# Kernel tuning notes

Hardware: AMD Instinct MI355X
Metric: run time of the kernel (lower is better)

Reference implementation:

```python
import jax, jax.numpy as jnp
import numpy as np

NUM_HEADS = 4
NUM_GROUPS = 8
EPS = 1e-5


def group_norm(x, w, b):
    # x: [B, C, H, W], 8 groups, per-channel affine
    B, C, H, W = x.shape
    g = x.reshape(B, NUM_GROUPS, C // NUM_GROUPS, H, W)
    mu = g.mean(axis=(2, 3, 4), keepdims=True)
    var = g.var(axis=(2, 3, 4), keepdims=True)
    g = (g - mu) * jax.lax.rsqrt(var + EPS)
    x = g.reshape(B, C, H, W)
    return x * w[None, :, None, None] + b[None, :, None, None]


def setup_inputs() -> dict:
    key = jax.random.key(0)
    ks = jax.random.split(key, 7)
    B, C, H, W = 16, 256, 32, 32
    x = jax.random.normal(ks[0], (B, C, H, W), dtype=jnp.float32)
    norm_w = jnp.ones((C,), jnp.float32)
    norm_b = jnp.zeros((C,), jnp.float32)
    # 1x1 convs == channel matmuls; fan-in scaled init
    qkv_w = jax.random.normal(ks[1], (3 * C, C), dtype=jnp.float32) / np.sqrt(C)
    qkv_b = jnp.zeros((3 * C,), jnp.float32)
    proj_w = jax.random.normal(ks[2], (C, C), dtype=jnp.float32) / np.sqrt(C)
    proj_b = jnp.zeros((C,), jnp.float32)
    return {"x": x, "norm_w": norm_w, "norm_b": norm_b,
            "qkv_w": qkv_w, "qkv_b": qkv_b,
            "proj_w": proj_w, "proj_b": proj_b}


def reference(x, norm_w, norm_b, qkv_w, qkv_b, proj_w, proj_b):
    B, C, H, W = x.shape
    nh = NUM_HEADS
    d = C // nh
    N = H * W

    h = group_norm(x, norm_w, norm_b)
    # 1x1 conv -> channel matmul: [B, 3C, H, W]
    qkv = jnp.einsum('oc,bchw->bohw', qkv_w, h) + qkv_b[None, :, None, None]
    qkv = qkv.reshape(B, 3, nh, d, N)
    q, k, v = qkv[:, 0], qkv[:, 1], qkv[:, 2]  # [B, nh, d, N]

    scale = d ** (-0.5)
    attn = jnp.einsum('bhcn,bhcm->bhnm', q, k) * scale  # [B, nh, N, N]
    attn = jax.nn.softmax(attn, axis=-1)
    out = jnp.einsum('bhnm,bhcm->bhcn', attn, v)  # [B, nh, d, N]
    out = out.reshape(B, C, H, W)
    out = jnp.einsum('oc,bchw->bohw', proj_w, out) + proj_b[None, :, None, None]
    return x + out
```

## Files before the change

kernel.cpp:

```cpp
#include <hip/hip_runtime.h>
#include <math.h>

#define BATCH 16
#define CH 256
#define NG 8
#define NH 4
#define HD 64
#define NN 1024
#define GSZ 32
#define GELEMS (GSZ * NN)

typedef __attribute__((ext_vector_type(8))) __bf16 bf16x8;
typedef __attribute__((ext_vector_type(4))) __bf16 bf16x4;
typedef __attribute__((ext_vector_type(4))) _Float16 f16x4;
typedef __attribute__((ext_vector_type(4))) float f32x4;

__device__ __forceinline__ unsigned short f2b(float f) {
    union { __bf16 h; unsigned short u; } c; c.h = (__bf16)f; return c.u;
}
__device__ __forceinline__ unsigned short f2h(float f) {
    union { _Float16 h; unsigned short u; } c; c.h = (_Float16)f; return c.u;
}

#define MFMA(a, b, c) __builtin_amdgcn_mfma_f32_16x16x32_bf16(a, b, c, 0, 0, 0)
#define MFMA16(a, b, c) __builtin_amdgcn_mfma_f32_16x16x16f16(a, b, c, 0, 0, 0)

__global__ __launch_bounds__(256) void gnw_kernel(
    const float* __restrict__ x, const float* __restrict__ w,
    const float* __restrict__ bb, const float* __restrict__ qkv_w,
    const float* __restrict__ proj_w, unsigned short* __restrict__ hT,
    unsigned short* __restrict__ wq, unsigned short* __restrict__ wp)
{
    int tid = threadIdx.x;
    if (blockIdx.x >= 128) {
        int t = (blockIdx.x - 128) * 256 + tid;
        const float* src; unsigned short* dst; size_t off;
        if (t < 24576) { src = qkv_w; dst = wq; off = (size_t)t * 8; }
        else           { src = proj_w; dst = wp; off = (size_t)(t - 24576) * 8; }
        const float4* s4 = (const float4*)(src + off);
        float4 a = s4[0], b = s4[1];
        bf16x8 pk;
        pk[0] = (__bf16)a.x; pk[1] = (__bf16)a.y; pk[2] = (__bf16)a.z; pk[3] = (__bf16)a.w;
        pk[4] = (__bf16)b.x; pk[5] = (__bf16)b.y; pk[6] = (__bf16)b.z; pk[7] = (__bf16)b.w;
        *(bf16x8*)(dst + off) = pk;
        return;
    }
    const int b = blockIdx.x >> 3, g = blockIdx.x & 7;
    const float* xb = x + ((size_t)b * CH + g * GSZ) * NN;
    const float4* x4 = (const float4*)xb;

    float s = 0.f, ss = 0.f;
    #pragma unroll
    for (int i = 0; i < 32; ++i) {
        float4 v = x4[tid + i * 256];
        s  += v.x + v.y + v.z + v.w;
        ss += v.x * v.x + v.y * v.y + v.z * v.z + v.w * v.w;
    }
    #pragma unroll
    for (int off = 1; off < 64; off <<= 1) {
        s  += __shfl_xor(s, off);
        ss += __shfl_xor(ss, off);
    }
    __shared__ float red[8];
    int wave = tid >> 6, lane = tid & 63;
    if (lane == 0) { red[wave] = s; red[4 + wave] = ss; }
    __syncthreads();
    if (tid == 0) {
        float ts  = red[0] + red[1] + red[2] + red[3];
        float tss = red[4] + red[5] + red[6] + red[7];
        float mu  = ts * (1.f / GELEMS);
        float var = tss * (1.f / GELEMS) - mu * mu;
        red[0] = mu; red[1] = rsqrtf(var + 1e-5f);
    }
    __syncthreads();
    const float mu = red[0], rs = red[1];

    const int co = tid & 3;
    float wcv[8], bcv[8];
    #pragma unroll
    for (int j = 0; j < 8; ++j) {
        int c = g * GSZ + co * 8 + j;
        wcv[j] = w[c] * rs;
        bcv[j] = bb[c] - mu * wcv[j];
    }
    __shared__ float Ts[32][66];
    const int cs = tid >> 3, q = tid & 7;
    const int n_l = tid >> 2;
    for (int nt = 0; nt < 16; ++nt) {
        const float2* src = (const float2*)(xb + (size_t)cs * NN + nt * 64 + q * 8);
        #pragma unroll
        for (int t = 0; t < 4; ++t)
            *(float2*)&Ts[cs][q * 8 + t * 2] = src[t];
        __syncthreads();
        bf16x8 pk;
        #pragma unroll
        for (int j = 0; j < 8; ++j)
            pk[j] = (__bf16)(Ts[co * 8 + j][n_l] * wcv[j] + bcv[j]);
        *(bf16x8*)(hT + ((size_t)b * NN + nt * 64 + n_l) * CH + g * GSZ + co * 8) = pk;
        __syncthreads();
    }
}

template <int KIND>
__global__ __launch_bounds__(256) void gemm_kernel(
    const unsigned short* __restrict__ AT,
    const unsigned short* __restrict__ Wb,
    const float* __restrict__ bias,
    unsigned short* __restrict__ outT, unsigned short* __restrict__ outV,
    const float* __restrict__ res, float* __restrict__ out)
{
    __shared__ __align__(16) unsigned short Ws[64][136];
    __shared__ __align__(16) unsigned short Hs[64][136];
    const int b = blockIdx.z, o0 = blockIdx.y * 64, n0 = blockIdx.x * 64;
    const int tid = threadIdx.x;
    const int lane = tid & 63, wv = tid >> 6;
    const int l = lane & 15, quad = lane >> 4;
    const int iw = wv & 1, jw = wv >> 1;
    const bool qk_mode = (KIND == 0) && (blockIdx.y < 8);
    const bool v_mode  = (KIND == 0) && (blockIdx.y >= 8);
    const int r4 = tid >> 2, c4 = tid & 3;

    f32x4 acc[2][2] = {};
    for (int st = 0; st < 2; ++st) {
        const int cc0 = st * 128;
        #pragma unroll
        for (int i = 0; i < 4; ++i) {
            int ch = c4 + i * 4;
            *(bf16x8*)&Ws[r4][ch * 8] =
                *(const bf16x8*)(Wb + (size_t)(o0 + r4) * CH + cc0 + ch * 8);
            *(bf16x8*)&Hs[r4][ch * 8] =
                *(const bf16x8*)(AT + ((size_t)b * NN + n0 + r4) * CH + cc0 + ch * 8);
        }
        __syncthreads();
        #pragma unroll
        for (int kt = 0; kt < 4; ++kt) {
            bf16x8 af[2], bf[2];
            #pragma unroll
            for (int i = 0; i < 2; ++i)
                af[i] = *(const bf16x8*)&Hs[iw * 32 + i * 16 + l][kt * 32 + quad * 8];
            #pragma unroll
            for (int j = 0; j < 2; ++j)
                bf[j] = *(const bf16x8*)&Ws[jw * 32 + j * 16 + l][kt * 32 + quad * 8];
            #pragma unroll
            for (int i = 0; i < 2; ++i)
                #pragma unroll
                for (int j = 0; j < 2; ++j)
                    acc[i][j] = v_mode ? MFMA(af[i], bf[j], acc[i][j])
                                       : MFMA(bf[j], af[i], acc[i][j]);
        }
        __syncthreads();
    }

    unsigned short* Cs = (unsigned short*)Ws;
    if (qk_mode) {
        #pragma unroll
        for (int i = 0; i < 2; ++i)
            #pragma unroll
            for (int j = 0; j < 2; ++j) {
                int o_p = jw * 32 + j * 16 + quad * 4;
                int n_l = iw * 32 + i * 16 + l;
                bf16x4 pk;
                #pragma unroll
                for (int r = 0; r < 4; ++r)
                    pk[r] = (__bf16)(acc[i][j][r] + bias[o0 + o_p + r]);
                *(bf16x4*)&Cs[n_l * 72 + o_p] = pk;
            }
        __syncthreads();
        int rr = tid >> 2, ch = tid & 3;
        bf16x8 a0 = *(const bf16x8*)&Cs[rr * 72 + ch * 16];
        bf16x8 a1 = *(const bf16x8*)&Cs[rr * 72 + ch * 16 + 8];
        unsigned short* dst = outT + ((size_t)b * NN + n0 + rr) * 512 + o0 + ch * 16;
        *(bf16x8*)dst = a0;
        *(bf16x8*)(dst + 8) = a1;
    } else if (v_mode) {
        #pragma unroll
        for (int i = 0; i < 2; ++i)
            #pragma unroll
            for (int j = 0; j < 2; ++j) {
                int n_p = iw * 32 + i * 16 + quad * 4;
                int o_l = jw * 32 + j * 16 + l;
                float bs = bias[o0 + o_l];
                f16x4 pk;
                #pragma unroll
                for (int r = 0; r < 4; ++r)
                    pk[r] = (_Float16)(acc[i][j][r] + bs);
                *(f16x4*)&Cs[o_l * 72 + n_p] = pk;
            }
        __syncthreads();
        int rr = tid >> 2, ch = tid & 3;
        bf16x8 a0 = *(const bf16x8*)&Cs[rr * 72 + ch * 16];
        bf16x8 a1 = *(const bf16x8*)&Cs[rr * 72 + ch * 16 + 8];
        unsigned short* dst = outV + ((size_t)b * CH + (o0 + rr - 512)) * NN + n0 + ch * 16;
        *(bf16x8*)dst = a0;
        *(bf16x8*)(dst + 8) = a1;
    } else {
        #pragma unroll
        for (int i = 0; i < 2; ++i)
            #pragma unroll
            for (int j = 0; j < 2; ++j) {
                int o = o0 + jw * 32 + j * 16 + quad * 4;
                int n = n0 + iw * 32 + i * 16 + l;
                #pragma unroll
                for (int r = 0; r < 4; ++r) {
                    size_t idx = ((size_t)b * CH + o + r) * NN + n;
                    out[idx] = acc[i][j][r] + bias[o + r] + res[idx];
                }
            }
    }
}

__global__ __launch_bounds__(256, 4) void attn_kernel(
    const unsigned short* __restrict__ qkvT,
    const unsigned short* __restrict__ vbuf,
    unsigned short* __restrict__ ctxT)
{
    __shared__ __align__(16) unsigned short KV[2][8192];
    __shared__ float Lred[2][32];
    const int id = blockIdx.x;
    const int bh = id & 63, nt = id >> 6;
    const int b = bh >> 2, hh = bh & 3;
    const int n0 = nt * 64;
    const int tid = threadIdx.x;
    const int lane = tid & 63, w = tid >> 6;
    const int l = lane & 15, quad = lane >> 4;
    const int qx = w & 1, ky = w >> 1;
    const float KL2E = 0.125f * 1.44269504f;
    const int r4 = tid >> 2, c4 = tid & 3;

    bf16x8 qf[2][2];
    {
        const unsigned short* qp = qkvT + ((size_t)b * NN + n0 + 32 * qx + l) * 512 + hh * 64;
        #pragma unroll
        for (int ns = 0; ns < 2; ++ns)
            #pragma unroll
            for (int kt = 0; kt < 2; ++kt)
                qf[ns][kt] = *(const bf16x8*)(qp + (size_t)ns * 16 * 512 + kt * 32 + quad * 8);
    }

    const unsigned short* gk = qkvT + ((size_t)b * NN + r4) * 512 + 256 + hh * 64;
    const unsigned short* gv = vbuf + ((size_t)b * CH + hh * 64 + r4) * NN;
    const int p0 = (c4 ^ (r4 & 7)) * 8, p1 = ((c4 + 4) ^ (r4 & 7)) * 8;

    bf16x8 kpre0, kpre1, vpre0, vpre1;
    kpre0 = *(const bf16x8*)(gk + c4 * 8);
    kpre1 = *(const bf16x8*)(gk + (c4 + 4) * 8);
    vpre0 = *(const bf16x8*)(gv + c4 * 8);
    vpre1 = *(const bf16x8*)(gv + (c4 + 4) * 8);
    *(bf16x8*)&KV[0][r4 * 64 + p0] = kpre0;
    *(bf16x8*)&KV[0][r4 * 64 + p1] = kpre1;
    *(bf16x8*)&KV[0][4096 + r4 * 64 + p0] = vpre0;
    *(bf16x8*)&KV[0][4096 + r4 * 64 + p1] = vpre1;
    __syncthreads();

    float l_w[2] = {0.f, 0.f};
    f32x4 oacc[2][4] = {};

    for (int mt = 0; mt < 16; ++mt) {
        const int cur = mt & 1;
        if (mt < 15) {
            const unsigned short* gk1 = gk + (size_t)(mt + 1) * 64 * 512;
            const unsigned short* gv1 = gv + (mt + 1) * 64;
            kpre0 = *(const bf16x8*)(gk1 + c4 * 8);
            kpre1 = *(const bf16x8*)(gk1 + (c4 + 4) * 8);
            vpre0 = *(const bf16x8*)(gv1 + c4 * 8);
            vpre1 = *(const bf16x8*)(gv1 + (c4 + 4) * 8);
        }

        bf16x8 kf[2][2];
        #pragma unroll
        for (int mt2 = 0; mt2 < 2; ++mt2)
            #pragma unroll
            for (int kt = 0; kt < 2; ++kt)
                kf[mt2][kt] = *(const bf16x8*)
                    &KV[cur][(32 * ky + 16 * mt2 + l) * 64 + (((kt * 4 + quad) ^ (l & 7)) * 8)];

        f32x4 sacc[2][2] = {};
        #pragma unroll
        for (int kt = 0; kt < 2; ++kt)
            #pragma unroll
            for (int mt2 = 0; mt2 < 2; ++mt2)
                #pragma unroll
                for (int ns = 0; ns < 2; ++ns)
                    sacc[mt2][ns] = MFMA(kf[mt2][kt], qf[ns][kt], sacc[mt2][ns]);

        f16x4 pf[2][2];
        #pragma unroll
        for (int mt2 = 0; mt2 < 2; ++mt2)
            #pragma unroll
            for (int ns = 0; ns < 2; ++ns)
                #pragma unroll
                for (int r = 0; r < 4; ++r) {
                    float p = exp2f(sacc[mt2][ns][r] * KL2E);
                    l_w[ns] += p;
                    pf[mt2][ns][r] = (_Float16)p;
                }

        #pragma unroll
        for (int mt2 = 0; mt2 < 2; ++mt2) {
            const int q8 = 4 * ky + 2 * mt2 + (quad >> 1);
            const int vo = ((q8 ^ (l & 7)) * 8) + (quad & 1) * 4;
            #pragma unroll
            for (int ct = 0; ct < 4; ++ct) {
                f16x4 va = *(const f16x4*)&KV[cur][4096 + (16 * ct + l) * 64 + vo];
                #pragma unroll
                for (int ns = 0; ns < 2; ++ns)
                    oacc[ns][ct] = MFMA16(va, pf[mt2][ns], oacc[ns][ct]);
            }
        }

        if (mt < 15) {
            const int nxt = cur ^ 1;
            *(bf16x8*)&KV[nxt][r4 * 64 + p0] = kpre0;
            *(bf16x8*)&KV[nxt][r4 * 64 + p1] = kpre1;
            *(bf16x8*)&KV[nxt][4096 + r4 * 64 + p0] = vpre0;
            *(bf16x8*)&KV[nxt][4096 + r4 * 64 + p1] = vpre1;
            __syncthreads();
        }
    }

    #pragma unroll
    for (int ns = 0; ns < 2; ++ns) {
        l_w[ns] += __shfl_xor(l_w[ns], 16);
        l_w[ns] += __shfl_xor(l_w[ns], 32);
    }
    float* Ored = (float*)&KV[0][0];
    if (ky == 1) {
        #pragma unroll
        for (int ns = 0; ns < 2; ++ns) {
            if (quad == 0) Lred[qx][ns * 16 + l] = l_w[ns];
            #pragma unroll
            for (int ct = 0; ct < 4; ++ct)
                #pragma unroll
                for (int r = 0; r < 4; ++r)
                    Ored[qx * 2048 + (16 * ct + quad * 4 + r) * 32 + ns * 16 + l] =
                        oacc[ns][ct][r];
        }
    }
    __syncthreads();
    if (ky == 0) {
        unsigned short* cb = ctxT + ((size_t)b * NN + n0 + 32 * qx) * CH + hh * 64;
        #pragma unroll
        for (int ns = 0; ns < 2; ++ns) {
            float inv = 1.f / (l_w[ns] + Lred[qx][ns * 16 + l]);
            #pragma unroll
            for (int ct = 0; ct < 4; ++ct) {
                bf16x4 pk;
                #pragma unroll
                for (int r = 0; r < 4; ++r)
                    pk[r] = (__bf16)((oacc[ns][ct][r] +
                             Ored[qx * 2048 + (16 * ct + quad * 4 + r) * 32 + ns * 16 + l]) * inv);
                *(bf16x4*)(cb + (size_t)(ns * 16 + l) * CH + 16 * ct + quad * 4) = pk;
            }
        }
    }
}

extern "C" void kernel_launch(void* const* d_in, const int* in_sizes, int n_in,
                              void* d_out, int out_size, void* d_ws, size_t ws_size,
                              hipStream_t stream)
{
    const float* x      = (const float*)d_in[0];
    const float* norm_w = (const float*)d_in[1];
    const float* norm_b = (const float*)d_in[2];
    const float* qkv_w  = (const float*)d_in[3];
    const float* qkv_b  = (const float*)d_in[4];
    const float* proj_w = (const float*)d_in[5];
    const float* proj_b = (const float*)d_in[6];
    float* out = (float*)d_out;

    unsigned short* hT   = (unsigned short*)d_ws;
    unsigned short* qkvT = hT   + (size_t)BATCH * NN * CH;
    unsigned short* vbuf = qkvT + (size_t)BATCH * NN * 512;
    unsigned short* ctxT = vbuf + (size_t)BATCH * CH * NN;
    unsigned short* wq   = ctxT + (size_t)BATCH * NN * CH;
    unsigned short* wp   = wq + (size_t)768 * CH;

    gnw_kernel<<<dim3(256), 256, 0, stream>>>(x, norm_w, norm_b, qkv_w, proj_w, hT, wq, wp);
    gemm_kernel<0><<<dim3(NN / 64, 12, BATCH), 256, 0, stream>>>(
        hT, wq, qkv_b, qkvT, vbuf, nullptr, nullptr);
    attn_kernel<<<dim3(1024), 256, 0, stream>>>(qkvT, vbuf, ctxT);
    gemm_kernel<1><<<dim3(NN / 64, 4, BATCH), 256, 0, stream>>>(
        ctxT, wp, proj_b, nullptr, nullptr, x, out);
}
```

Before: 145.8 us.

## Fold softmax scale into Q, remap QKV GEMM blocks, widen group-norm loads

Multiplies the Q projection output by scale*log2(e) in the QKV GEMM epilogue so the attention kernel drops a multiply per score before exp2. Changes the QKV GEMM to a 1D grid with a block-index mapping that interleaves batches, likely aimed at L2/XCD locality of weights and activations. Switches the group-norm staging loads from float2 to float4 and pads the shared tile to 68 columns. Rounding Q to bf16 after scaling slightly changes the numerics.

```diff
diff --git a/kernel.cpp b/kernel.cpp
--- a/kernel.cpp
+++ b/kernel.cpp
@@ -18,12 +18,10 @@
 __device__ __forceinline__ unsigned short f2b(float f) {
     union { __bf16 h; unsigned short u; } c; c.h = (__bf16)f; return c.u;
 }
-__device__ __forceinline__ unsigned short f2h(float f) {
-    union { _Float16 h; unsigned short u; } c; c.h = (_Float16)f; return c.u;
-}
 
 #define MFMA(a, b, c) __builtin_amdgcn_mfma_f32_16x16x32_bf16(a, b, c, 0, 0, 0)
 #define MFMA16(a, b, c) __builtin_amdgcn_mfma_f32_16x16x16f16(a, b, c, 0, 0, 0)
+#define KL2E 0.1803368801111204f
 
 __global__ __launch_bounds__(256) void gnw_kernel(
     const float* __restrict__ x, const float* __restrict__ w,
@@ -83,14 +81,13 @@
         wcv[j] = w[c] * rs;
         bcv[j] = bb[c] - mu * wcv[j];
     }
-    __shared__ float Ts[32][66];
+    __shared__ float Ts[32][68];
     const int cs = tid >> 3, q = tid & 7;
     const int n_l = tid >> 2;
     for (int nt = 0; nt < 16; ++nt) {
-        const float2* src = (const float2*)(xb + (size_t)cs * NN + nt * 64 + q * 8);
-        #pragma unroll
-        for (int t = 0; t < 4; ++t)
-            *(float2*)&Ts[cs][q * 8 + t * 2] = src[t];
+        const float4* src = (const float4*)(xb + (size_t)cs * NN + nt * 64 + q * 8);
+        *(float4*)&Ts[cs][q * 8]     = src[0];
+        *(float4*)&Ts[cs][q * 8 + 4] = src[1];
         __syncthreads();
         bf16x8 pk;
         #pragma unroll
@@ -109,17 +106,27 @@
     unsigned short* __restrict__ outT, unsigned short* __restrict__ outV,
     const float* __restrict__ res, float* __restrict__ out)
 {
-    __shared__ __align__(16) unsigned short Ws[64][136];
-    __shared__ __align__(16) unsigned short Hs[64][136];
-    const int b = blockIdx.z, o0 = blockIdx.y * 64, n0 = blockIdx.x * 64;
+    int b, yy, xx;
+    if (KIND == 0) {
+        const int id = blockIdx.x;
+        b = (id & 7) + ((id >= 1536) ? 8 : 0);
+        const int rem = (id >> 3) % 192;
+        yy = rem % 12;
+        xx = rem / 12;
+    } else {
+        b = blockIdx.z; yy = blockIdx.y; xx = blockIdx.x;
+    }
+    const int o0 = yy * 64, n0 = xx * 64;
     const int tid = threadIdx.x;
     const int lane = tid & 63, wv = tid >> 6;
     const int l = lane & 15, quad = lane >> 4;
     const int iw = wv & 1, jw = wv >> 1;
-    const bool qk_mode = (KIND == 0) && (blockIdx.y < 8);
-    const bool v_mode  = (KIND == 0) && (blockIdx.y >= 8);
+    const bool qk_mode = (KIND == 0) && (yy < 8);
+    const bool v_mode  = (KIND == 0) && (yy >= 8);
     const int r4 = tid >> 2, c4 = tid & 3;
 
+    __shared__ __align__(16) unsigned short Ws[64][136];
+    __shared__ __align__(16) unsigned short Hs[64][136];
     f32x4 acc[2][2] = {};
     for (int st = 0; st < 2; ++st) {
         const int cc0 = st * 128;
@@ -153,6 +160,7 @@
 
     unsigned short* Cs = (unsigned short*)Ws;
     if (qk_mode) {
+        const float qs = (o0 < 256) ? KL2E : 1.f;
         #pragma unroll
         for (int i = 0; i < 2; ++i)
             #pragma unroll
@@ -162,7 +170,7 @@
                 bf16x4 pk;
                 #pragma unroll
                 for (int r = 0; r < 4; ++r)
-                    pk[r] = (__bf16)(acc[i][j][r] + bias[o0 + o_p + r]);
+                    pk[r] = (__bf16)((acc[i][j][r] + bias[o0 + o_p + r]) * qs);
                 *(bf16x4*)&Cs[n_l * 72 + o_p] = pk;
             }
         __syncthreads();
@@ -224,7 +232,6 @@
     const int lane = tid & 63, w = tid >> 6;
     const int l = lane & 15, quad = lane >> 4;
     const int qx = w & 1, ky = w >> 1;
-    const float KL2E = 0.125f * 1.44269504f;
     const int r4 = tid >> 2, c4 = tid & 3;
 
     bf16x8 qf[2][2];
@@ -290,7 +297,7 @@
             for (int ns = 0; ns < 2; ++ns)
                 #pragma unroll
                 for (int r = 0; r < 4; ++r) {
-                    float p = exp2f(sacc[mt2][ns][r] * KL2E);
+                    float p = exp2f(sacc[mt2][ns][r]);
                     l_w[ns] += p;
                     pf[mt2][ns][r] = (_Float16)p;
                 }
@@ -376,9 +383,9 @@
     unsigned short* wp   = wq + (size_t)768 * CH;
 
     gnw_kernel<<<dim3(256), 256, 0, stream>>>(x, norm_w, norm_b, qkv_w, proj_w, hT, wq, wp);
-    gemm_kernel<0><<<dim3(NN / 64, 12, BATCH), 256, 0, stream>>>(
+    gemm_kernel<0><<<dim3(3072), 256, 0, stream>>>(
         hT, wq, qkv_b, qkvT, vbuf, nullptr, nullptr);
     attn_kernel<<<dim3(1024), 256, 0, stream>>>(qkvT, vbuf, ctxT);
-    gemm_kernel<1><<<dim3(NN / 64, 4, BATCH), 256, 0, stream>>>(
+    gemm_kernel<1><<<dim3(16, 4, BATCH), 256, 0, stream>>>(
         ctxT, wp, proj_b, nullptr, nullptr, x, out);
 }
```

Measured after the change: 146.8 us. About the same (+0.6%).
